# Performance work log

Hardware: AMD Instinct MI355X
Metric: run time of the kernel (lower is better)

## Reference

```python
import jax, jax.numpy as jnp
import numpy as np

VOCAB, EMBED, HIDDEN, NCLS = 50257, 64, 64, 5
B, S = 4096, 512
BN_EPS = 1e-5


def setup_inputs() -> dict:
    key = jax.random.key(0)
    ks = jax.random.split(key, 10)
    x = jax.random.randint(ks[0], (B, S), 0, VOCAB, dtype=jnp.int64 if jax.config.jax_enable_x64 else jnp.int32)
    emb = jax.random.normal(ks[1], (VOCAB, EMBED), dtype=jnp.float32)
    emb = emb.at[0].set(0.0)  # padding_idx=0
    s = 1.0 / np.sqrt(HIDDEN)
    W_ih = jax.random.uniform(ks[2], (HIDDEN, EMBED), minval=-s, maxval=s, dtype=jnp.float32)
    W_hh = jax.random.uniform(ks[3], (HIDDEN, HIDDEN), minval=-s, maxval=s, dtype=jnp.float32)
    b_ih = jax.random.uniform(ks[4], (HIDDEN,), minval=-s, maxval=s, dtype=jnp.float32)
    b_hh = jax.random.uniform(ks[5], (HIDDEN,), minval=-s, maxval=s, dtype=jnp.float32)
    gamma = jnp.ones((HIDDEN,), dtype=jnp.float32)
    beta = jnp.zeros((HIDDEN,), dtype=jnp.float32)
    sf = 1.0 / np.sqrt(HIDDEN)
    W_fc = jax.random.uniform(ks[6], (NCLS, HIDDEN), minval=-sf, maxval=sf, dtype=jnp.float32)
    b_fc = jax.random.uniform(ks[7], (NCLS,), minval=-sf, maxval=sf, dtype=jnp.float32)
    return {"x": x, "emb": emb, "W_ih": W_ih, "W_hh": W_hh, "b_ih": b_ih,
            "b_hh": b_hh, "gamma": gamma, "beta": beta, "W_fc": W_fc, "b_fc": b_fc}


def reference(x, emb, W_ih, W_hh, b_ih, b_hh, gamma, beta, W_fc, b_fc):
    # embedding gather: [B, S, E]
    xe = emb[x]
    # precompute input projection once: [B, S, H] -> scan over time as [S, B, H]
    xp = jnp.einsum('bse,he->bsh', xe, W_ih) + b_ih + b_hh
    xp_t = jnp.swapaxes(xp, 0, 1)

    def step(h, xt):
        h = jnp.tanh(xt + h @ W_hh.T)
        return h, None

    h0 = jnp.zeros((x.shape[0], HIDDEN), dtype=xp.dtype)
    h_n, _ = jax.lax.scan(step, h0, xp_t)

    # BatchNorm1d (training-mode math: batch stats, biased variance)
    mean = jnp.mean(h_n, axis=0)
    var = jnp.mean((h_n - mean) ** 2, axis=0)
    h_bn = (h_n - mean) * jax.lax.rsqrt(var + BN_EPS) * gamma + beta
    # dropout is identity in eval / deterministic reference
    logits = h_bn @ W_fc.T + b_fc  # [B, 5]
    return logits
```

## Files before the change

kernel.cpp:

```cpp
#include <hip/hip_runtime.h>

typedef unsigned short u16;
typedef __attribute__((ext_vector_type(8))) short bf16x8;
typedef __attribute__((ext_vector_type(4))) float f32x4;
typedef __attribute__((ext_vector_type(4))) u16 u16x4;

constexpr int BATCH = 4096;
constexpr int SEQ   = 512;
constexpr int HID   = 64;

__device__ __forceinline__ float bf2f(u16 u) {
  union { unsigned int i; float f; } c; c.i = ((unsigned int)u) << 16; return c.f;
}
__device__ __forceinline__ u16 f2bf(float f) {
  union { float f; unsigned int i; } c; c.f = f;
  unsigned int u = c.i;
  u += 0x7fffu + ((u >> 16) & 1u);
  return (u16)(u >> 16);
}

#define MFMA16(a, b, c) __builtin_amdgcn_mfma_f32_16x16x32_bf16(a, b, c, 0, 0, 0)

__global__ __launch_bounds__(256) void cvt_emb_kernel(
    const float4* __restrict__ src, u16x4* __restrict__ dst, int n4)
{
  int i = blockIdx.x * 256 + threadIdx.x;
  if (i < n4) {
    float4 v = src[i];
    u16x4 o;
    o.x = f2bf(v.x); o.y = f2bf(v.y); o.z = f2bf(v.z); o.w = f2bf(v.w);
    dst[i] = o;
  }
}

__global__ __launch_bounds__(256) void cvt_w_kernel(
    const float* __restrict__ Wih, const float* __restrict__ Whh,
    u16* __restrict__ wih_hi, u16* __restrict__ whh_hi, u16* __restrict__ whh_lo)
{
  int i = blockIdx.x * 256 + threadIdx.x;
  wih_hi[i] = f2bf(Wih[i]);
  float w = Whh[i];
  u16 hi = f2bf(w);
  whh_hi[i] = hi;
  whh_lo[i] = f2bf(w - bf2f(hi));
}

__global__ __launch_bounds__(256) void rnn_scan_kernel(
    const int* __restrict__ xx, const u16* __restrict__ emb_bf,
    const u16* __restrict__ wih_hi, const u16* __restrict__ whh_hi,
    const u16* __restrict__ whh_lo,
    const float* __restrict__ b_ih, const float* __restrict__ b_hh,
    float* __restrict__ hT )
{
  __shared__ u16 hbuf[2 * 2048];
  const int tid = threadIdx.x;
  const int w = tid >> 6;
  const int L = tid & 63;
  const int n = L & 15;
  const int q = L >> 4;
  const int R0 = blockIdx.x << 4;
  const int row  = R0 + n;
  const int feat = (w << 4) + n;

  ((int4*)hbuf)[tid] = int4{0, 0, 0, 0};

  bf16x8 Bih0 = *(const bf16x8*)(wih_hi + feat * 64 +      8 * q);
  bf16x8 Bih1 = *(const bf16x8*)(wih_hi + feat * 64 + 32 + 8 * q);
  bf16x8 Bh0  = *(const bf16x8*)(whh_hi + feat * 64 +      8 * q);
  bf16x8 Bh1  = *(const bf16x8*)(whh_hi + feat * 64 + 32 + 8 * q);
  bf16x8 Bl0  = *(const bf16x8*)(whh_lo + feat * 64 +      8 * q);
  bf16x8 Bl1  = *(const bf16x8*)(whh_lo + feat * 64 + 32 + 8 * q);
  const float bias = b_ih[feat] + b_hh[feat];

  const int r0off = n * 64 + (((0 + q) ^ (n & 7)) << 3);
  const int r1off = n * 64 + (((4 + q) ^ (n & 7)) << 3);
  const int cwbase = (w << 1) + (n >> 3);

  const int4* x4 = (const int4*)(xx + row * SEQ);
  int4 K0 = x4[0];
  int4 K1 = x4[1];

  bf16x8 e0[2], e1[2];
  {
    const u16* eb = emb_bf + (long)K0.x * 64 + 8 * q;
    e0[0] = *(const bf16x8*)(eb);
    e1[0] = *(const bf16x8*)(eb + 32);
    eb = emb_bf + (long)K0.y * 64 + 8 * q;
    e0[1] = *(const bf16x8*)(eb);
    e1[1] = *(const bf16x8*)(eb + 32);
  }

  __syncthreads();

  for (int t = 0; t < SEQ / 4; ++t) {
    const int tt = (t + 2 < SEQ / 4) ? t + 2 : SEQ / 4 - 1;
    int4 K2 = x4[tt];
    const int nid[4] = {K0.z, K0.w, K1.x, K1.y};

    #pragma unroll
    for (int u = 0; u < 4; ++u) {
      const int p = u & 1;
      const u16* hb = hbuf + p * 2048;
      bf16x8 ah0 = *(const bf16x8*)(hb + r0off);
      bf16x8 ah1 = *(const bf16x8*)(hb + r1off);
      bf16x8 al0 = *(const bf16x8*)(hb + 1024 + r0off);
      bf16x8 al1 = *(const bf16x8*)(hb + 1024 + r1off);

      f32x4 C1 = {bias, bias, bias, bias};
      C1 = MFMA16(e0[p], Bih0, C1);
      C1 = MFMA16(e1[p], Bih1, C1);

      {
        const u16* eb = emb_bf + (long)nid[u] * 64 + 8 * q;
        e0[p] = *(const bf16x8*)(eb);
        e1[p] = *(const bf16x8*)(eb + 32);
      }

      f32x4 Cx = {0.f, 0.f, 0.f, 0.f};
      f32x4 Cy = {0.f, 0.f, 0.f, 0.f};
      f32x4 Cz = {0.f, 0.f, 0.f, 0.f};
      Cx = MFMA16(ah0, Bh0, Cx);  Cx = MFMA16(al0, Bh0, Cx);
      Cy = MFMA16(ah1, Bh1, Cy);  Cy = MFMA16(al1, Bh1, Cy);
      Cz = MFMA16(ah0, Bl0, Cz);  Cz = MFMA16(ah1, Bl1, Cz);

      u16* wb = hbuf + (p ^ 1) * 2048;
      const bool last = (t == SEQ / 4 - 1) && (u == 3);
      #pragma unroll
      for (int r = 0; r < 4; ++r) {
        float v = C1[r] + ((Cx[r] + Cy[r]) + Cz[r]);
        float ex = __expf(v + v);
        float th = fmaf(-2.0f, __builtin_amdgcn_rcpf(ex + 1.0f), 1.0f);
        const int mw = (q << 2) + r;
        const int off = mw * 64 + ((cwbase ^ (mw & 7)) << 3) + (n & 7);
        unsigned int tb = __float_as_uint(th);
        u16 hi = (u16)(tb >> 16);
        float rem = th - __uint_as_float(tb & 0xffff0000u);
        wb[off] = hi;
        wb[1024 + off] = (u16)(__float_as_uint(rem) >> 16);
        if (last) hT[feat * BATCH + R0 + mw] = th;
      }
      asm volatile("s_waitcnt lgkmcnt(0)\n\ts_barrier" ::: "memory");
    }
    K0 = K1; K1 = K2;
  }
}

__global__ __launch_bounds__(256) void bn_stats_kernel(
    const float* __restrict__ hT, const float* __restrict__ gamma,
    const float* __restrict__ beta, float* __restrict__ scale_shift)
{
  const int j = blockIdx.x;
  const float* v = hT + j * BATCH;
  float sum = 0.f, sq = 0.f;
  for (int i = threadIdx.x; i < BATCH; i += 256) {
    float t = v[i];
    sum += t;
    sq = fmaf(t, t, sq);
  }
  #pragma unroll
  for (int o = 32; o > 0; o >>= 1) {
    sum += __shfl_down(sum, o, 64);
    sq  += __shfl_down(sq,  o, 64);
  }
  __shared__ float s1[4], s2[4];
  const int wv = threadIdx.x >> 6;
  if ((threadIdx.x & 63) == 0) { s1[wv] = sum; s2[wv] = sq; }
  __syncthreads();
  if (threadIdx.x == 0) {
    float S1 = s1[0] + s1[1] + s1[2] + s1[3];
    float S2 = s2[0] + s2[1] + s2[2] + s2[3];
    float mean = S1 * (1.0f / BATCH);
    float var  = S2 * (1.0f / BATCH) - mean * mean;
    float inv  = rsqrtf(var + 1e-5f);
    float sc   = gamma[j] * inv;
    scale_shift[j]      = sc;
    scale_shift[64 + j] = beta[j] - mean * sc;
  }
}

__global__ __launch_bounds__(256) void head_kernel(
    const float* __restrict__ hT, const float* __restrict__ scale_shift,
    const float* __restrict__ Wfc, const float* __restrict__ bfc,
    float* __restrict__ out)
{
  const int b = blockIdx.x * 256 + threadIdx.x;
  float acc[5];
  #pragma unroll
  for (int c = 0; c < 5; ++c) acc[c] = bfc[c];
  for (int j = 0; j < HID; ++j) {
    float hv  = hT[j * BATCH + b];
    float hat = fmaf(hv, scale_shift[j], scale_shift[64 + j]);
    #pragma unroll
    for (int c = 0; c < 5; ++c) acc[c] = fmaf(hat, Wfc[c * 64 + j], acc[c]);
  }
  #pragma unroll
  for (int c = 0; c < 5; ++c) out[b * 5 + c] = acc[c];
}

extern "C" void kernel_launch(void* const* d_in, const int* in_sizes, int n_in,
                              void* d_out, int out_size, void* d_ws, size_t ws_size,
                              hipStream_t stream)
{
  const int*   x     = (const int*)d_in[0];
  const float* emb   = (const float*)d_in[1];
  const float* W_ih  = (const float*)d_in[2];
  const float* W_hh  = (const float*)d_in[3];
  const float* b_ih  = (const float*)d_in[4];
  const float* b_hh  = (const float*)d_in[5];
  const float* gamma = (const float*)d_in[6];
  const float* beta  = (const float*)d_in[7];
  const float* W_fc  = (const float*)d_in[8];
  const float* b_fc  = (const float*)d_in[9];

  char* ws = (char*)d_ws;
  float* hT          = (float*)ws;
  float* scale_shift = (float*)(ws + 1048576);
  u16*   emb_bf      = (u16*)(ws + 1049088);
  u16*   wih_hi      = (u16*)(ws + 7481984);
  u16*   whh_hi      = (u16*)(ws + 7490176);
  u16*   whh_lo      = (u16*)(ws + 7498368);

  const int emb_n4 = 50257 * 64 / 4;
  cvt_emb_kernel<<<dim3((emb_n4 + 255) / 256), dim3(256), 0, stream>>>(
      (const float4*)emb, (u16x4*)emb_bf, emb_n4);
  cvt_w_kernel<<<dim3(16), dim3(256), 0, stream>>>(
      W_ih, W_hh, wih_hi, whh_hi, whh_lo);
  rnn_scan_kernel<<<dim3(BATCH / 16), dim3(256), 0, stream>>>(
      x, emb_bf, wih_hi, whh_hi, whh_lo, b_ih, b_hh, hT);
  bn_stats_kernel<<<dim3(HID), dim3(256), 0, stream>>>(hT, gamma, beta, scale_shift);
  head_kernel<<<dim3(BATCH / 256), dim3(256), 0, stream>>>(
      hT, scale_shift, W_fc, b_fc, (float*)d_out);
}
```

Baseline: 277.3 us.

## Fuse prep kernels, fold BN stats into scan epilogue, deepen embedding prefetch

```diff
diff --git a/kernel.cpp b/kernel.cpp
--- a/kernel.cpp
+++ b/kernel.cpp
@@ -5,9 +5,10 @@
 typedef __attribute__((ext_vector_type(4))) float f32x4;
 typedef __attribute__((ext_vector_type(4))) u16 u16x4;
 
-constexpr int BATCH = 4096;
-constexpr int SEQ   = 512;
-constexpr int HID   = 64;
+constexpr int BATCH  = 4096;
+constexpr int SEQ    = 512;
+constexpr int HID    = 64;
+constexpr int EMB_N4 = 50257 * 64 / 4;
 
 __device__ __forceinline__ float bf2f(u16 u) {
   union { unsigned int i; float f; } c; c.i = ((unsigned int)u) << 16; return c.f;
@@ -21,36 +22,40 @@
 
 #define MFMA16(a, b, c) __builtin_amdgcn_mfma_f32_16x16x32_bf16(a, b, c, 0, 0, 0)
 
-__global__ __launch_bounds__(256) void cvt_emb_kernel(
-    const float4* __restrict__ src, u16x4* __restrict__ dst, int n4)
-{
-  int i = blockIdx.x * 256 + threadIdx.x;
-  if (i < n4) {
-    float4 v = src[i];
+__global__ __launch_bounds__(256) void prep_kernel(
+    const float4* __restrict__ emb4, const float* __restrict__ Wih,
+    const float* __restrict__ Whh, u16x4* __restrict__ emb_bf4,
+    u16* __restrict__ wih_hi, u16* __restrict__ whh_hi, u16* __restrict__ whh_lo,
+    float* __restrict__ bn_acc)
+{
+  int gid = blockIdx.x * 256 + threadIdx.x;
+  if (gid < EMB_N4) {
+    float4 v = emb4[gid];
     u16x4 o;
     o.x = f2bf(v.x); o.y = f2bf(v.y); o.z = f2bf(v.z); o.w = f2bf(v.w);
-    dst[i] = o;
-  }
-}
-
-__global__ __launch_bounds__(256) void cvt_w_kernel(
-    const float* __restrict__ Wih, const float* __restrict__ Whh,
-    u16* __restrict__ wih_hi, u16* __restrict__ whh_hi, u16* __restrict__ whh_lo)
-{
-  int i = blockIdx.x * 256 + threadIdx.x;
-  wih_hi[i] = f2bf(Wih[i]);
-  float w = Whh[i];
-  u16 hi = f2bf(w);
-  whh_hi[i] = hi;
-  whh_lo[i] = f2bf(w - bf2f(hi));
-}
-
-__global__ __launch_bounds__(256) void rnn_scan_kernel(
+    emb_bf4[gid] = o;
+  } else if (gid < EMB_N4 + 1024) {
+    int i0 = (gid - EMB_N4) * 4;
+    #pragma unroll
+    for (int k = 0; k < 4; ++k) {
+      int i = i0 + k;
+      wih_hi[i] = f2bf(Wih[i]);
+      float w = Whh[i];
+      u16 hi = f2bf(w);
+      whh_hi[i] = hi;
+      whh_lo[i] = f2bf(w - bf2f(hi));
+    }
+  } else if (gid < EMB_N4 + 1024 + 128) {
+    bn_acc[gid - (EMB_N4 + 1024)] = 0.f;
+  }
+}
+
+__global__ __launch_bounds__(256, 1) void rnn_scan_kernel(
     const int* __restrict__ xx, const u16* __restrict__ emb_bf,
     const u16* __restrict__ wih_hi, const u16* __restrict__ whh_hi,
     const u16* __restrict__ whh_lo,
     const float* __restrict__ b_ih, const float* __restrict__ b_hh,
-    float* __restrict__ hT )
+    float* __restrict__ hT , float* __restrict__ bn_acc)
 {
   __shared__ u16 hbuf[2 * 2048];
   const int tid = threadIdx.x;
@@ -77,25 +82,26 @@
   const int cwbase = (w << 1) + (n >> 3);
 
   const int4* x4 = (const int4*)(xx + row * SEQ);
-  int4 K0 = x4[0];
   int4 K1 = x4[1];
 
-  bf16x8 e0[2], e1[2];
+  bf16x8 e0[4], e1[4];
   {
-    const u16* eb = emb_bf + (long)K0.x * 64 + 8 * q;
-    e0[0] = *(const bf16x8*)(eb);
-    e1[0] = *(const bf16x8*)(eb + 32);
-    eb = emb_bf + (long)K0.y * 64 + 8 * q;
-    e0[1] = *(const bf16x8*)(eb);
-    e1[1] = *(const bf16x8*)(eb + 32);
+    int4 K0 = x4[0];
+    const int id0[4] = {K0.x, K0.y, K0.z, K0.w};
+    #pragma unroll
+    for (int u = 0; u < 4; ++u) {
+      const u16* eb = emb_bf + (long)id0[u] * 64 + 8 * q;
+      e0[u] = *(const bf16x8*)(eb);
+      e1[u] = *(const bf16x8*)(eb + 32);
+    }
   }
 
   __syncthreads();
 
   for (int t = 0; t < SEQ / 4; ++t) {
-    const int tt = (t + 2 < SEQ / 4) ? t + 2 : SEQ / 4 - 1;
-    int4 K2 = x4[tt];
-    const int nid[4] = {K0.z, K0.w, K1.x, K1.y};
+    int4 K2 = x4[(t + 2 < SEQ / 4) ? t + 2 : SEQ / 4 - 1];
+    const int nid[4] = {K1.x, K1.y, K1.z, K1.w};
+    const bool lastt = (t == SEQ / 4 - 1);
 
     #pragma unroll
     for (int u = 0; u < 4; ++u) {
@@ -107,13 +113,13 @@
       bf16x8 al1 = *(const bf16x8*)(hb + 1024 + r1off);
 
       f32x4 C1 = {bias, bias, bias, bias};
-      C1 = MFMA16(e0[p], Bih0, C1);
-      C1 = MFMA16(e1[p], Bih1, C1);
+      C1 = MFMA16(e0[u], Bih0, C1);
+      C1 = MFMA16(e1[u], Bih1, C1);
 
       {
         const u16* eb = emb_bf + (long)nid[u] * 64 + 8 * q;
-        e0[p] = *(const bf16x8*)(eb);
-        e1[p] = *(const bf16x8*)(eb + 32);
+        e0[u] = *(const bf16x8*)(eb);
+        e1[u] = *(const bf16x8*)(eb + 32);
       }
 
       f32x4 Cx = {0.f, 0.f, 0.f, 0.f};
@@ -124,72 +130,66 @@
       Cz = MFMA16(ah0, Bl0, Cz);  Cz = MFMA16(ah1, Bl1, Cz);
 
       u16* wb = hbuf + (p ^ 1) * 2048;
-      const bool last = (t == SEQ / 4 - 1) && (u == 3);
+      float th4[4];
       #pragma unroll
       for (int r = 0; r < 4; ++r) {
-        float v = C1[r] + ((Cx[r] + Cy[r]) + Cz[r]);
-        float ex = __expf(v + v);
+        float v = (C1[r] + Cx[r]) + (Cy[r] + Cz[r]);
+        float ex = __builtin_amdgcn_exp2f(2.8853900817779268f * v);
         float th = fmaf(-2.0f, __builtin_amdgcn_rcpf(ex + 1.0f), 1.0f);
+        th4[r] = th;
         const int mw = (q << 2) + r;
         const int off = mw * 64 + ((cwbase ^ (mw & 7)) << 3) + (n & 7);
         unsigned int tb = __float_as_uint(th);
-        u16 hi = (u16)(tb >> 16);
-        float rem = th - __uint_as_float(tb & 0xffff0000u);
-        wb[off] = hi;
-        wb[1024 + off] = (u16)(__float_as_uint(rem) >> 16);
-        if (last) hT[feat * BATCH + R0 + mw] = th;
+        wb[off] = (u16)(tb >> 16);
+        wb[1024 + off] = (u16)(__float_as_uint(th - __uint_as_float(tb & 0xffff0000u)) >> 16);
       }
+
+      if (u == 3 && lastt) {
+        float s1 = 0.f, s2 = 0.f;
+        #pragma unroll
+        for (int r = 0; r < 4; ++r) {
+          hT[feat * BATCH + R0 + (q << 2) + r] = th4[r];
+          s1 += th4[r];
+          s2 = fmaf(th4[r], th4[r], s2);
+        }
+        s1 += __shfl_xor(s1, 16, 64);  s2 += __shfl_xor(s2, 16, 64);
+        s1 += __shfl_xor(s1, 32, 64);  s2 += __shfl_xor(s2, 32, 64);
+        if (q == 0) {
+          atomicAdd(bn_acc + feat, s1);
+          atomicAdd(bn_acc + 64 + feat, s2);
+        }
+      }
+
       asm volatile("s_waitcnt lgkmcnt(0)\n\ts_barrier" ::: "memory");
     }
-    K0 = K1; K1 = K2;
-  }
-}
-
-__global__ __launch_bounds__(256) void bn_stats_kernel(
-    const float* __restrict__ hT, const float* __restrict__ gamma,
-    const float* __restrict__ beta, float* __restrict__ scale_shift)
-{
-  const int j = blockIdx.x;
-  const float* v = hT + j * BATCH;
-  float sum = 0.f, sq = 0.f;
-  for (int i = threadIdx.x; i < BATCH; i += 256) {
-    float t = v[i];
-    sum += t;
-    sq = fmaf(t, t, sq);
-  }
-  #pragma unroll
-  for (int o = 32; o > 0; o >>= 1) {
-    sum += __shfl_down(sum, o, 64);
-    sq  += __shfl_down(sq,  o, 64);
-  }
-  __shared__ float s1[4], s2[4];
-  const int wv = threadIdx.x >> 6;
-  if ((threadIdx.x & 63) == 0) { s1[wv] = sum; s2[wv] = sq; }
-  __syncthreads();
-  if (threadIdx.x == 0) {
-    float S1 = s1[0] + s1[1] + s1[2] + s1[3];
-    float S2 = s2[0] + s2[1] + s2[2] + s2[3];
-    float mean = S1 * (1.0f / BATCH);
-    float var  = S2 * (1.0f / BATCH) - mean * mean;
-    float inv  = rsqrtf(var + 1e-5f);
-    float sc   = gamma[j] * inv;
-    scale_shift[j]      = sc;
-    scale_shift[64 + j] = beta[j] - mean * sc;
+    K1 = K2;
   }
 }
 
 __global__ __launch_bounds__(256) void head_kernel(
-    const float* __restrict__ hT, const float* __restrict__ scale_shift,
+    const float* __restrict__ hT, const float* __restrict__ bn_acc,
+    const float* __restrict__ gamma, const float* __restrict__ beta,
     const float* __restrict__ Wfc, const float* __restrict__ bfc,
     float* __restrict__ out)
 {
-  const int b = blockIdx.x * 256 + threadIdx.x;
+  __shared__ float sc[64], sh[64];
+  const int tid = threadIdx.x;
+  if (tid < 64) {
+    float mean = bn_acc[tid] * (1.0f / BATCH);
+    float var  = bn_acc[64 + tid] * (1.0f / BATCH) - mean * mean;
+    float inv  = rsqrtf(var + 1e-5f);
+    float s    = gamma[tid] * inv;
+    sc[tid] = s;
+    sh[tid] = beta[tid] - mean * s;
+  }
+  __syncthreads();
+  const int b = blockIdx.x * 256 + tid;
   float acc[5];
   #pragma unroll
   for (int c = 0; c < 5; ++c) acc[c] = bfc[c];
   for (int j = 0; j < HID; ++j) {
     float hv  = hT[j * BATCH + b];
-    float hat = fmaf(hv, scale_shift[j], scale_shift[64 + j]);
+    float hat = fmaf(hv, sc[j], sh[j]);
     #pragma unroll
     for (int c = 0; c < 5; ++c) acc[c] = fmaf(hat, Wfc[c * 64 + j], acc[c]);
   }
@@ -213,21 +213,18 @@
   const float* b_fc  = (const float*)d_in[9];
 
   char* ws = (char*)d_ws;
-  float* hT          = (float*)ws;
-  float* scale_shift = (float*)(ws + 1048576);
-  u16*   emb_bf      = (u16*)(ws + 1049088);
-  u16*   wih_hi      = (u16*)(ws + 7481984);
-  u16*   whh_hi      = (u16*)(ws + 7490176);
-  u16*   whh_lo      = (u16*)(ws + 7498368);
-
-  const int emb_n4 = 50257 * 64 / 4;
-  cvt_emb_kernel<<<dim3((emb_n4 + 255) / 256), dim3(256), 0, stream>>>(
-      (const float4*)emb, (u16x4*)emb_bf, emb_n4);
-  cvt_w_kernel<<<dim3(16), dim3(256), 0, stream>>>(
-      W_ih, W_hh, wih_hi, whh_hi, whh_lo);
+  float* hT     = (float*)ws;
+  float* bn_acc = (float*)(ws + 1048576);
+  u16*   emb_bf = (u16*)(ws + 1049088);
+  u16*   wih_hi = (u16*)(ws + 7481984);
+  u16*   whh_hi = (u16*)(ws + 7490176);
+  u16*   whh_lo = (u16*)(ws + 7498368);
+
+  const int prep_items = EMB_N4 + 1024 + 128;
+  prep_kernel<<<dim3((prep_items + 255) / 256), dim3(256), 0, stream>>>(
+      (const float4*)emb, W_ih, W_hh, (u16x4*)emb_bf, wih_hi, whh_hi, whh_lo, bn_acc);
   rnn_scan_kernel<<<dim3(BATCH / 16), dim3(256), 0, stream>>>(
-      x, emb_bf, wih_hi, whh_hi, whh_lo, b_ih, b_hh, hT);
-  bn_stats_kernel<<<dim3(HID), dim3(256), 0, stream>>>(hT, gamma, beta, scale_shift);
+      x, emb_bf, wih_hi, whh_hi, whh_lo, b_ih, b_hh, hT, bn_acc);
   head_kernel<<<dim3(BATCH / 256), dim3(256), 0, stream>>>(
-      hT, scale_shift, W_fc, b_fc, (float*)d_out);
-}
+      hT, bn_acc, gamma, beta, W_fc, b_fc, (float*)d_out);
+}
```

Result: faster. 250.7 us (-9.6%).
